# Optimization experiments

Hardware: AMD Instinct MI355X
Metric: run time of the kernel (lower is better)

The kernel has to match this reference:

```python
import jax, jax.numpy as jnp
import numpy as np

D_MODEL = 1024
D_STATE = 16
D_CONV = 4
EXPAND = 2
DT_RANK = 64
D_INNER = EXPAND * D_MODEL  # 2048
BATCH = 2
SEQ = 1024


def _silu(v):
    return v * jax.nn.sigmoid(v)


def setup_inputs() -> dict:
    key = jax.random.key(0)
    ks = jax.random.split(key, 8)
    x = jax.random.normal(ks[0], (BATCH, SEQ, D_MODEL), dtype=jnp.float32)
    W_in = jax.random.normal(ks[1], (2 * D_INNER, D_MODEL), dtype=jnp.float32) * (D_MODEL ** -0.5)
    conv_w = jax.random.normal(ks[2], (D_INNER, 1, D_CONV), dtype=jnp.float32) * (D_CONV ** -0.5)
    conv_b = jnp.zeros((D_INNER,), dtype=jnp.float32)
    W_x = jax.random.normal(ks[3], (DT_RANK + 2 * D_STATE, D_INNER), dtype=jnp.float32) * (D_INNER ** -0.5)
    W_dt = jax.random.uniform(ks[4], (D_INNER, DT_RANK), minval=-(DT_RANK ** -0.5), maxval=DT_RANK ** -0.5, dtype=jnp.float32)
    # dt bias init: inverse-softplus of dt sampled log-uniform in [1e-3, 1e-1]
    dt = jnp.exp(jax.random.uniform(ks[5], (D_INNER,), dtype=jnp.float32) * (np.log(0.1) - np.log(0.001)) + np.log(0.001))
    dt = jnp.clip(dt, 1e-4)
    b_dt = dt + jnp.log(-jnp.expm1(-dt))
    # A_log init: log of 1..d_state tiled per channel (S4D-real)
    A_log = jnp.log(jnp.tile(jnp.arange(1, D_STATE + 1, dtype=jnp.float32), (D_INNER, 1)))
    D = jnp.ones((D_INNER,), dtype=jnp.float32)
    W_out = jax.random.normal(ks[6], (D_MODEL, D_INNER), dtype=jnp.float32) * (D_INNER ** -0.5)
    return {"x": x, "W_in": W_in, "conv_w": conv_w, "conv_b": conv_b, "W_x": W_x,
            "W_dt": W_dt, "b_dt": b_dt, "A_log": A_log, "D": D, "W_out": W_out}


def _selective_scan(u, dt, A, B_in, C_in, D):
    # u, dt: [B,L,d_inner]; B_in, C_in: [B,L,d_state]; A: [d_inner,d_state]; D: [d_inner]
    Bsz = u.shape[0]

    def step(h, inp):
        u_t, dt_t, B_t, C_t = inp  # [B,d_inner], [B,d_inner], [B,d_state], [B,d_state]
        dA = jnp.exp(dt_t[:, :, None] * A)                     # [B,d_inner,d_state]
        h = dA * h + dt_t[:, :, None] * B_t[:, None, :] * u_t[:, :, None]
        y = jnp.einsum('bds,bs->bd', h, C_t)
        return h, y

    h0 = jnp.zeros((Bsz, D_INNER, D_STATE), dtype=u.dtype)
    xs = (u.transpose(1, 0, 2), dt.transpose(1, 0, 2),
          B_in.transpose(1, 0, 2), C_in.transpose(1, 0, 2))
    _, ys = jax.lax.scan(step, h0, xs)                          # ys: [L,B,d_inner]
    return ys.transpose(1, 0, 2) + u * D


def reference(x, W_in, conv_w, conv_b, W_x, W_dt, b_dt, A_log, D, W_out):
    # in_proj and gate split
    xz = x @ W_in.T                                            # [B,T,2*d_inner]
    x_in, z = jnp.split(xz, 2, axis=-1)
    # depthwise causal conv1d (left-pad d_conv-1, same as pad-both + slice :T)
    xi = x_in.transpose(0, 2, 1)                               # [B,d_inner,T]
    conv = jax.lax.conv_general_dilated(xi, conv_w, window_strides=(1,),
                                        padding=[(D_CONV - 1, 0)],
                                        feature_group_count=D_INNER)
    x_act = _silu(conv + conv_b[None, :, None]).transpose(0, 2, 1)  # [B,T,d_inner]
    # dt / B / C projections
    dbc = x_act @ W_x.T
    dt_lr, B_in, C_in = jnp.split(dbc, [DT_RANK, DT_RANK + D_STATE], axis=-1)
    dt = jax.nn.softplus(dt_lr @ W_dt.T + b_dt)                # [B,T,d_inner]
    A = -jnp.exp(A_log)                                        # [d_inner,d_state]
    y = _selective_scan(x_act, dt, A, B_in, C_in, D)
    y = y * _silu(z)
    return y @ W_out.T
```

## Files before the change

kernel.cpp:

```cpp
#include <hip/hip_runtime.h>
#include <math.h>

#define D_MODEL 1024
#define D_STATE 16
#define D_CONV  4
#define DT_RANK 64
#define D_INNER 2048
#define BATCH   2
#define SEQ     1024
#define BT      (BATCH*SEQ)
#define KSPLIT  16

typedef int   v4i __attribute__((ext_vector_type(4)));
typedef float v4f __attribute__((ext_vector_type(4)));
typedef short s8v __attribute__((ext_vector_type(8)));
typedef unsigned short u16;

template<int BM, int BN, int BK, int TM, int TN, int EPI>
__launch_bounds__(256)
__global__ void gemm_nt(const float* __restrict__ A, int lda,
                        const float* __restrict__ B, int ldb,
                        float* __restrict__ C, int ldc,
                        int K, const float* __restrict__ bias) {
    constexpr int BX = BN / TN;
    constexpr int BY = BM / TM;
    constexpr int THREADS = BX * BY;

    __shared__ float As[BK][BM + 1];
    __shared__ float Bs[BK][BN + 1];

    const int tid = threadIdx.x;
    const int tx  = tid % BX;
    const int ty  = tid / BX;
    const int m0  = blockIdx.y * BM;
    const int n0  = blockIdx.x * BN;

    float acc[TM][TN] = {};

    for (int k0 = 0; k0 < K; k0 += BK) {
        #pragma unroll
        for (int l = 0; l < (BM * BK) / (THREADS * 4); ++l) {
            int idx = (tid + l * THREADS) * 4;
            int row = idx / BK, col = idx % BK;
            const float4 v = *reinterpret_cast<const float4*>(
                &A[(size_t)(m0 + row) * lda + k0 + col]);
            As[col + 0][row] = v.x; As[col + 1][row] = v.y;
            As[col + 2][row] = v.z; As[col + 3][row] = v.w;
        }
        #pragma unroll
        for (int l = 0; l < (BN * BK) / (THREADS * 4); ++l) {
            int idx = (tid + l * THREADS) * 4;
            int row = idx / BK, col = idx % BK;
            const float4 v = *reinterpret_cast<const float4*>(
                &B[(size_t)(n0 + row) * ldb + k0 + col]);
            Bs[col + 0][row] = v.x; Bs[col + 1][row] = v.y;
            Bs[col + 2][row] = v.z; Bs[col + 3][row] = v.w;
        }
        __syncthreads();

        #pragma unroll
        for (int kk = 0; kk < BK; ++kk) {
            float a[TM], b[TN];
            #pragma unroll
            for (int i = 0; i < TM; ++i) a[i] = As[kk][ty * TM + i];
            #pragma unroll
            for (int j = 0; j < TN; ++j) b[j] = Bs[kk][tx * TN + j];
            #pragma unroll
            for (int i = 0; i < TM; ++i)
                #pragma unroll
                for (int j = 0; j < TN; ++j)
                    acc[i][j] = fmaf(a[i], b[j], acc[i][j]);
        }
        __syncthreads();
    }

    #pragma unroll
    for (int i = 0; i < TM; ++i) {
        float* outp = &C[(size_t)(m0 + ty * TM + i) * ldc + n0 + tx * TN];
        float vals[4];
        #pragma unroll
        for (int j = 0; j < TN; ++j) {
            float val = acc[i][j];
            if (EPI == 1) {
                val += bias[n0 + tx * TN + j];
                val = (val > 20.f) ? val : log1pf(expf(val));
            }
            vals[j] = val;
        }
        float4 v;
        v.x = vals[0]; v.y = vals[1]; v.z = vals[2]; v.w = vals[3];
        *reinterpret_cast<float4*>(outp) = v;
    }
}

template<int BM, int BN, int BK, int TM, int TN>
__launch_bounds__(128)
__global__ void gemm_nt_splitk(const float* __restrict__ A, int lda,
                               const float* __restrict__ B, int ldb,
                               float* __restrict__ part, int N, int kchunk) {
    constexpr int BX = BN / TN;
    constexpr int BY = BM / TM;
    constexpr int THREADS = BX * BY;

    __shared__ float As[BK][BM + 1];
    __shared__ float Bs[BK][BN + 1];

    const int tid = threadIdx.x;
    const int tx  = tid % BX;
    const int ty  = tid / BX;
    const int m0  = blockIdx.y * BM;
    const int n0  = blockIdx.x * BN;
    const int kb  = blockIdx.z * kchunk;

    float acc[TM][TN] = {};

    for (int k0 = kb; k0 < kb + kchunk; k0 += BK) {
        #pragma unroll
        for (int l = 0; l < (BM * BK) / (THREADS * 4); ++l) {
            int idx = (tid + l * THREADS) * 4;
            int row = idx / BK, col = idx % BK;
            const float4 v = *reinterpret_cast<const float4*>(
                &A[(size_t)(m0 + row) * lda + k0 + col]);
            As[col + 0][row] = v.x; As[col + 1][row] = v.y;
            As[col + 2][row] = v.z; As[col + 3][row] = v.w;
        }
        #pragma unroll
        for (int l = 0; l < (BN * BK) / (THREADS * 4); ++l) {
            int idx = (tid + l * THREADS) * 4;
            int row = idx / BK, col = idx % BK;
            const float4 v = *reinterpret_cast<const float4*>(
                &B[(size_t)(n0 + row) * ldb + k0 + col]);
            Bs[col + 0][row] = v.x; Bs[col + 1][row] = v.y;
            Bs[col + 2][row] = v.z; Bs[col + 3][row] = v.w;
        }
        __syncthreads();

        #pragma unroll
        for (int kk = 0; kk < BK; ++kk) {
            float a[TM], b[TN];
            #pragma unroll
            for (int i = 0; i < TM; ++i) a[i] = As[kk][ty * TM + i];
            #pragma unroll
            for (int j = 0; j < TN; ++j) b[j] = Bs[kk][tx * TN + j];
            #pragma unroll
            for (int i = 0; i < TM; ++i)
                #pragma unroll
                for (int j = 0; j < TN; ++j)
                    acc[i][j] = fmaf(a[i], b[j], acc[i][j]);
        }
        __syncthreads();
    }

    float* base = part + (size_t)blockIdx.z * BT * N;
    #pragma unroll
    for (int i = 0; i < TM; ++i) {
        float* outp = &base[(size_t)(m0 + ty * TM + i) * N + n0 + tx * TN];
        float4 v;
        v.x = acc[i][0]; v.y = acc[i][1]; v.z = acc[i][2]; v.w = acc[i][3];
        *reinterpret_cast<float4*>(outp) = v;
    }
}

__global__ void reduce_splitk(const float* __restrict__ part,
                              float* __restrict__ outp, int n) {
    const int idx = blockIdx.x * 256 + threadIdx.x;
    if (idx >= n) return;
    float s = 0.f;
    #pragma unroll
    for (int kc = 0; kc < KSPLIT; ++kc)
        s += part[(size_t)kc * n + idx];
    outp[idx] = s;
}

__device__ __forceinline__ u16 rne_bf16(float x) {
    unsigned int u = __float_as_uint(x);
    unsigned int r = u + 0x7FFFu + ((u >> 16) & 1u);
    return (u16)(r >> 16);
}

__global__ void prep_kernel(const float* __restrict__ x,
                            const float* __restrict__ Win,
                            const float* __restrict__ Wout,
                            u16* __restrict__ xh,
                            u16* __restrict__ winh, u16* __restrict__ wouth) {
    const size_t M2 = 2u * 1024u * 1024u;
    size_t i = ((size_t)blockIdx.x * 256 + threadIdx.x) * 8;
    const float* src;
    u16* dst;
    size_t j;
    if (i < M2)            { src = x;    dst = xh;    j = i; }
    else if (i < 3 * M2)   { src = Win;  dst = winh;  j = i - M2; }
    else                   { src = Wout; dst = wouth; j = i - 3 * M2; }
    float4 a = *reinterpret_cast<const float4*>(&src[j]);
    float4 b = *reinterpret_cast<const float4*>(&src[j + 4]);
    float xs[8] = {a.x, a.y, a.z, a.w, b.x, b.y, b.z, b.w};
    unsigned int hw[4];
    #pragma unroll
    for (int q = 0; q < 4; ++q)
        hw[q] = (unsigned int)rne_bf16(xs[2*q]) | ((unsigned int)rne_bf16(xs[2*q+1]) << 16);
    *reinterpret_cast<v4i*>(&dst[j]) = *reinterpret_cast<v4i*>(hw);
}

template<int BM, int BN, int WM, int WN>
__launch_bounds__(256)
__global__ void gemm_bf16(const u16* __restrict__ Ahi, int lda,
                          const u16* __restrict__ Bhi, int ldb,
                          float* __restrict__ C, int ldc, int K) {
    constexpr int ACH = BM / 64;
    constexpr int BCH = BN / 64;
    constexpr int WMF = WM / 16;
    constexpr int WNF = WN / 16;
    constexpr int SA  = BM * 40;
    constexpr int SB  = BN * 40;
    constexpr int BUFSZ = SA + SB;
    constexpr int WCOLS = BN / WN;

    __shared__ u16 smem[2 * BUFSZ];

    const int tid  = threadIdx.x;
    const int lane = tid & 63;
    const int wave = tid >> 6;
    const int wr   = wave / WCOLS, wc = wave % WCOLS;
    const int m0   = blockIdx.y * BM, n0 = blockIdx.x * BN;

    size_t aBase[ACH]; int aW[ACH];
    #pragma unroll
    for (int q = 0; q < ACH; ++q) {
        int c = tid + q * 256, row = c >> 2, slot = c & 3;
        aBase[q] = (size_t)(m0 + row) * lda + slot * 8;
        aW[q] = row * 40 + slot * 8;
    }
    size_t bBase[BCH]; int bW[BCH];
    #pragma unroll
    for (int q = 0; q < BCH; ++q) {
        int c = tid + q * 256, row = c >> 2, slot = c & 3;
        bBase[q] = (size_t)(n0 + row) * ldb + slot * 8;
        bW[q] = row * 40 + slot * 8;
    }

    const int fr = lane & 15;
    const int fk = (lane >> 4) * 8;
    const int fq = lane >> 4;
    int aOff[WMF], bOff[WNF];
    #pragma unroll
    for (int i = 0; i < WMF; ++i) aOff[i] = (wr * WM + i * 16 + fr) * 40 + fk;
    #pragma unroll
    for (int j = 0; j < WNF; ++j) bOff[j] = (wc * WN + j * 16 + fr) * 40 + fk;

    v4f acc[WMF][WNF];
    #pragma unroll
    for (int i = 0; i < WMF; ++i)
        #pragma unroll
        for (int j = 0; j < WNF; ++j)
            acc[i][j] = (v4f)0.f;

    v4i rA[ACH], rB[BCH];

    auto loadg = [&](int k0) {
        #pragma unroll
        for (int q = 0; q < ACH; ++q)
            rA[q] = *reinterpret_cast<const v4i*>(Ahi + aBase[q] + k0);
        #pragma unroll
        for (int q = 0; q < BCH; ++q)
            rB[q] = *reinterpret_cast<const v4i*>(Bhi + bBase[q] + k0);
    };
    auto writelds = [&](u16* buf) {
        #pragma unroll
        for (int q = 0; q < ACH; ++q)
            *reinterpret_cast<v4i*>(&buf[aW[q]]) = rA[q];
        #pragma unroll
        for (int q = 0; q < BCH; ++q)
            *reinterpret_cast<v4i*>(&buf[SA + bW[q]]) = rB[q];
    };

    const int NK = K / 32;
    loadg(0);
    writelds(smem);
    if (NK > 1) loadg(32);
    __syncthreads();

    for (int k = 0; k < NK; ++k) {
        u16* cur = smem + (k & 1) * BUFSZ;
        if (k + 1 < NK) {
            writelds(smem + ((k + 1) & 1) * BUFSZ);
            if (k + 2 < NK) loadg((k + 2) * 32);
        }

        s8v ah[WMF];
        #pragma unroll
        for (int i = 0; i < WMF; ++i)
            ah[i] = *reinterpret_cast<const s8v*>(&cur[aOff[i]]);
        #pragma unroll
        for (int j = 0; j < WNF; ++j) {
            const s8v bh = *reinterpret_cast<const s8v*>(&cur[SA + bOff[j]]);
            #pragma unroll
            for (int i = 0; i < WMF; ++i)
                acc[i][j] = __builtin_amdgcn_mfma_f32_16x16x32_bf16(ah[i], bh, acc[i][j], 0, 0, 0);
        }
        __syncthreads();
    }

    #pragma unroll
    for (int i = 0; i < WMF; ++i) {
        const int row = m0 + wr * WM + i * 16 + fq * 4;
        #pragma unroll
        for (int j = 0; j < WNF; ++j) {
            const int col = n0 + wc * WN + j * 16 + fr;
            #pragma unroll
            for (int r = 0; r < 4; ++r)
                C[(size_t)(row + r) * ldc + col] = acc[i][j][r];
        }
    }
}

__global__ void conv_silu_kernel(const float* __restrict__ x_in, int xld,
                                 const float* __restrict__ w,
                                 const float* __restrict__ b,
                                 float* __restrict__ x_act) {
    const int idx = blockIdx.x * blockDim.x + threadIdx.x;
    const int ch4 = (idx * 4) % D_INNER;
    const int m   = (idx * 4) / D_INNER;
    const int t   = m % SEQ;

    float4 wrow[4];
    #pragma unroll
    for (int c = 0; c < 4; ++c)
        wrow[c] = *reinterpret_cast<const float4*>(&w[(ch4 + c) * D_CONV]);
    float4 acc = *reinterpret_cast<const float4*>(&b[ch4]);

    #pragma unroll
    for (int j = 0; j < D_CONV; ++j) {
        const int tt = t - (D_CONV - 1) + j;
        if (tt >= 0) {
            const float4 xi = *reinterpret_cast<const float4*>(
                &x_in[(size_t)(m - (D_CONV - 1) + j) * xld + ch4]);
            acc.x = fmaf(((const float*)&wrow[0])[j], xi.x, acc.x);
            acc.y = fmaf(((const float*)&wrow[1])[j], xi.y, acc.y);
            acc.z = fmaf(((const float*)&wrow[2])[j], xi.z, acc.z);
            acc.w = fmaf(((const float*)&wrow[3])[j], xi.w, acc.w);
        }
    }
    acc.x = acc.x / (1.f + __expf(-acc.x));
    acc.y = acc.y / (1.f + __expf(-acc.y));
    acc.z = acc.z / (1.f + __expf(-acc.z));
    acc.w = acc.w / (1.f + __expf(-acc.w));
    *reinterpret_cast<float4*>(&x_act[(size_t)idx * 4]) = acc;
}

template<int NC>
__launch_bounds__(256)
__global__ void scan_part1(const float* __restrict__ dt,
                           const float* __restrict__ x_act,
                           const float* __restrict__ dbc,
                           const float* __restrict__ A_log,
                           float* __restrict__ P, float* __restrict__ F) {
    constexpr int CL = SEQ / NC;
    __shared__ float Bsh[CL][D_STATE];
    const int tid = threadIdx.x;
    const int d = blockIdx.x * 256 + tid;
    const int c = blockIdx.y;
    const int b = blockIdx.z;
    const int mbase = b * SEQ + c * CL;

    {
        const int s = tid & 15, t0 = tid >> 4;
        #pragma unroll
        for (int q = 0; q < CL / 16; ++q)
            Bsh[t0 + 16 * q][s] = dbc[(size_t)(mbase + t0 + 16 * q) * 96 + DT_RANK + s];
    }
    float A[16];
    #pragma unroll
    for (int q = 0; q < 4; ++q) {
        float4 v = *reinterpret_cast<const float4*>(&A_log[d * 16 + q * 4]);
        A[q*4+0] = -__expf(v.x); A[q*4+1] = -__expf(v.y);
        A[q*4+2] = -__expf(v.z); A[q*4+3] = -__expf(v.w);
    }
    __syncthreads();

    float h[16] = {};
    float Pp[16];
    #pragma unroll
    for (int s = 0; s < 16; ++s) Pp[s] = 1.f;

    for (int t = 0; t < CL; ++t) {
        const int m = mbase + t;
        const float dtv = dt[(size_t)m * D_INNER + d];
        const float u   = x_act[(size_t)m * D_INNER + d];
        const float du  = dtv * u;
        float Bv[16];
        #pragma unroll
        for (int q = 0; q < 4; ++q) {
            float4 v = *reinterpret_cast<const float4*>(&Bsh[t][q * 4]);
            Bv[q*4+0] = v.x; Bv[q*4+1] = v.y; Bv[q*4+2] = v.z; Bv[q*4+3] = v.w;
        }
        #pragma unroll
        for (int s = 0; s < 16; ++s) {
            const float dA = __expf(dtv * A[s]);
            Pp[s] *= dA;
            h[s] = fmaf(dA, h[s], du * Bv[s]);
        }
    }
    const size_t base = ((size_t)(b * NC + c) * 16) * D_INNER + d;
    #pragma unroll
    for (int s = 0; s < 16; ++s) {
        P[base + (size_t)s * D_INNER] = Pp[s];
        F[base + (size_t)s * D_INNER] = h[s];
    }
}

template<int NC>
__launch_bounds__(256, 2)
__global__ void scan_combine(const float* __restrict__ P, float* F) {
    const int idx = blockIdx.x * 256 + threadIdx.x;
    const int d  = idx % D_INNER;
    const int bs = idx / D_INNER;
    const int b  = bs >> 4, s = bs & 15;
    const size_t base0 = ((size_t)b * NC * 16 + s) * D_INNER + d;
    const size_t cstep = (size_t)16 * D_INNER;

    float Pv[NC], Fv[NC];
    #pragma unroll
    for (int c = 0; c < NC; ++c) {
        Pv[c] = P[base0 + c * cstep];
        Fv[c] = F[base0 + c * cstep];
    }
    float G = 0.f;
    #pragma unroll
    for (int c = 0; c < NC; ++c) {
        const float f = Fv[c];
        Fv[c] = G;
        G = fmaf(Pv[c], G, f);
    }
    #pragma unroll
    for (int c = 0; c < NC; ++c)
        F[base0 + c * cstep] = Fv[c];
}

template<int NC, int BF16OUT>
__launch_bounds__(256)
__global__ void scan_part2(const float* __restrict__ dt,
                           const float* __restrict__ x_act,
                           const float* __restrict__ dbc,
                           const float* __restrict__ A_log,
                           const float* __restrict__ Dp,
                           const float* __restrict__ Ginit,
                           const float* zp, int zld,
                           float* yf, u16* yh) {
    constexpr int CL = SEQ / NC;
    __shared__ float BCs[CL][32];
    const int tid = threadIdx.x;
    const int d = blockIdx.x * 256 + tid;
    const int c = blockIdx.y;
    const int b = blockIdx.z;
    const int mbase = b * SEQ + c * CL;

    {
        const int t0 = tid >> 3;
        const int j  = (tid & 7) * 4;
        if (t0 < CL) {
            float4 v = *reinterpret_cast<const float4*>(
                &dbc[(size_t)(mbase + t0) * 96 + DT_RANK + j]);
            *reinterpret_cast<float4*>(&BCs[t0][j]) = v;
        }
    }
    float A[16];
    #pragma unroll
    for (int q = 0; q < 4; ++q) {
        float4 v = *reinterpret_cast<const float4*>(&A_log[d * 16 + q * 4]);
        A[q*4+0] = -__expf(v.x); A[q*4+1] = -__expf(v.y);
        A[q*4+2] = -__expf(v.z); A[q*4+3] = -__expf(v.w);
    }
    float h[16];
    const size_t gbase = ((size_t)(b * NC + c) * 16) * D_INNER + d;
    #pragma unroll
    for (int s = 0; s < 16; ++s) h[s] = Ginit[gbase + (size_t)s * D_INNER];
    const float Dv = Dp[d];
    __syncthreads();

    for (int half = 0; half < 2; ++half) {
        const int tb = half * (CL / 2);
        float zreg[CL / 2];
        #pragma unroll
        for (int t = 0; t < CL / 2; ++t)
            zreg[t] = zp[(size_t)(mbase + tb + t) * zld + d];

        for (int t = 0; t < CL / 2; ++t) {
            const int m = mbase + tb + t;
            const float dtv = dt[(size_t)m * D_INNER + d];
            const float u   = x_act[(size_t)m * D_INNER + d];
            const float du  = dtv * u;
            float Bv[16], Cv[16];
            #pragma unroll
            for (int q = 0; q < 4; ++q) {
                float4 vb = *reinterpret_cast<const float4*>(&BCs[tb + t][q * 4]);
                float4 vc = *reinterpret_cast<const float4*>(&BCs[tb + t][16 + q * 4]);
                Bv[q*4+0] = vb.x; Bv[q*4+1] = vb.y; Bv[q*4+2] = vb.z; Bv[q*4+3] = vb.w;
                Cv[q*4+0] = vc.x; Cv[q*4+1] = vc.y; Cv[q*4+2] = vc.z; Cv[q*4+3] = vc.w;
            }
            float y0 = 0.f, y1 = 0.f;
            #pragma unroll
            for (int s = 0; s < 16; s += 2) {
                const float dA0 = __expf(dtv * A[s]);
                const float dA1 = __expf(dtv * A[s + 1]);
                h[s]     = fmaf(dA0, h[s],     du * Bv[s]);
                h[s + 1] = fmaf(dA1, h[s + 1], du * Bv[s + 1]);
                y0 = fmaf(h[s],     Cv[s],     y0);
                y1 = fmaf(h[s + 1], Cv[s + 1], y1);
            }
            float y = y0 + y1;
            y = fmaf(u, Dv, y);
            const float zv = zreg[t];
            const float g  = zv / (1.f + __expf(-zv));
            const float val = y * g;
            if (BF16OUT) {
                yh[(size_t)m * D_INNER + d] = rne_bf16(val);
            } else {
                yf[(size_t)m * D_INNER + d] = val;
            }
        }
    }
}

extern "C" void kernel_launch(void* const* d_in, const int* in_sizes, int n_in,
                              void* d_out, int out_size, void* d_ws, size_t ws_size,
                              hipStream_t stream) {
    const float* x      = (const float*)d_in[0];
    const float* W_in   = (const float*)d_in[1];
    const float* conv_w = (const float*)d_in[2];
    const float* conv_b = (const float*)d_in[3];
    const float* W_x    = (const float*)d_in[4];
    const float* W_dt   = (const float*)d_in[5];
    const float* b_dt   = (const float*)d_in[6];
    const float* A_log  = (const float*)d_in[7];
    const float* Dp     = (const float*)d_in[8];
    const float* W_out  = (const float*)d_in[9];
    float* out = (float*)d_out;

    const size_t M1 = 1024u * 1024u;
    const size_t fXZ = 8 * M1, fXACT = 4 * M1, fDBC = (size_t)BT * 96,
                 fDT = 4 * M1;
    const size_t fPF32 = 2 * M1;
    const size_t fPF64 = 4 * M1;
    const size_t shorts = 12 * M1;
    const size_t need32 = (fXZ + fXACT + fDBC + fDT + 2 * fPF32) * 4 + shorts * 2;
    const size_t need64 = (fXZ + fXACT + fDBC + fDT + 2 * fPF64) * 4 + shorts * 2;

    if (ws_size >= need32) {
        const bool big = (ws_size >= need64);
        const size_t fPF = big ? fPF64 : fPF32;

        float* ws    = (float*)d_ws;
        float* xz    = ws;
        float* x_act = xz    + fXZ;
        float* dbc   = x_act + fXACT;
        float* dtbuf = dbc   + fDBC;
        float* Pbuf  = dtbuf + fDT;
        float* Fbuf  = Pbuf  + fPF;
        u16* xh    = (u16*)(Fbuf + fPF);
        u16* winh  = xh    + 2 * M1;
        u16* wouth = winh  + 4 * M1;
        u16* yh    = wouth + 2 * M1;
        float* dbc_part = Pbuf;

        prep_kernel<<<dim3((8 * M1) / 2048), 256, 0, stream>>>(
            x, W_in, W_out, xh, winh, wouth);

        gemm_bf16<128, 128, 64, 64><<<dim3(4096 / 128, BT / 128), 256, 0, stream>>>(
            xh, D_MODEL, winh, D_MODEL, xz, 4096, D_MODEL);

        conv_silu_kernel<<<dim3((BT * D_INNER) / 1024), 256, 0, stream>>>(
            xz, 4096, conv_w, conv_b, x_act);

        gemm_nt_splitk<64,32,16,4,4><<<dim3(96 / 32, BT / 64, KSPLIT), 128, 0, stream>>>(
            x_act, D_INNER, W_x, D_INNER, dbc_part, 96, D_INNER / KSPLIT);
        reduce_splitk<<<dim3((BT * 96 + 255) / 256), 256, 0, stream>>>(
            dbc_part, dbc, BT * 96);

        gemm_nt<64,64,16,4,4,1><<<dim3(D_INNER / 64, BT / 64), 256, 0, stream>>>(
            dbc, 96, W_dt, DT_RANK, dtbuf, D_INNER, DT_RANK, b_dt);

        if (big) {
            scan_part1<64><<<dim3(D_INNER / 256, 64, BATCH), 256, 0, stream>>>(
                dtbuf, x_act, dbc, A_log, Pbuf, Fbuf);
            scan_combine<64><<<dim3((BATCH * 16 * D_INNER) / 256), 256, 0, stream>>>(
                Pbuf, Fbuf);
            scan_part2<64, 1><<<dim3(D_INNER / 256, 64, BATCH), 256, 0, stream>>>(
                dtbuf, x_act, dbc, A_log, Dp, Fbuf, xz + D_INNER, 4096,
                nullptr, yh);
        } else {
            scan_part1<32><<<dim3(D_INNER / 256, 32, BATCH), 256, 0, stream>>>(
                dtbuf, x_act, dbc, A_log, Pbuf, Fbuf);
            scan_combine<32><<<dim3((BATCH * 16 * D_INNER) / 256), 256, 0, stream>>>(
                Pbuf, Fbuf);
            scan_part2<32, 1><<<dim3(D_INNER / 256, 32, BATCH), 256, 0, stream>>>(
                dtbuf, x_act, dbc, A_log, Dp, Fbuf, xz + D_INNER, 4096,
                nullptr, yh);
        }

        gemm_bf16<64, 128, 32, 64><<<dim3(D_MODEL / 128, BT / 64), 256, 0, stream>>>(
            yh, D_INNER, wouth, D_INNER, out, D_MODEL, D_INNER);
    } else {
        float* ws    = (float*)d_ws;
        float* x_in  = ws;
        float* z     = x_in  + (size_t)BT * D_INNER;
        float* x_act = z     + (size_t)BT * D_INNER;
        float* dbc   = x_act + (size_t)BT * D_INNER;
        float* Pbuf  = dbc   + (size_t)BT * 96;
        float* Fbuf  = Pbuf  + (size_t)BATCH * 32 * 16 * D_INNER;
        float* dtbuf = x_in;
        float* yf    = z;

        gemm_nt<64,64,16,4,4,0><<<dim3(D_INNER/64, BT/64), 256, 0, stream>>>(
            x, D_MODEL, W_in, D_MODEL, x_in, D_INNER, D_MODEL, nullptr);
        gemm_nt<64,64,16,4,4,0><<<dim3(D_INNER/64, BT/64), 256, 0, stream>>>(
            x, D_MODEL, W_in + (size_t)D_INNER * D_MODEL, D_MODEL, z, D_INNER, D_MODEL, nullptr);
        conv_silu_kernel<<<dim3((BT * D_INNER) / 1024), 256, 0, stream>>>(
            x_in, D_INNER, conv_w, conv_b, x_act);
        gemm_nt<64,32,16,4,4,0><<<dim3(96/32, BT/64), 128, 0, stream>>>(
            x_act, D_INNER, W_x, D_INNER, dbc, 96, D_INNER, nullptr);
        gemm_nt<64,64,16,4,4,1><<<dim3(D_INNER/64, BT/64), 256, 0, stream>>>(
            dbc, 96, W_dt, DT_RANK, dtbuf, D_INNER, DT_RANK, b_dt);
        scan_part1<32><<<dim3(D_INNER/256, 32, BATCH), 256, 0, stream>>>(
            dtbuf, x_act, dbc, A_log, Pbuf, Fbuf);
        scan_combine<32><<<dim3((BATCH * 16 * D_INNER) / 256), 256, 0, stream>>>(
            Pbuf, Fbuf);
        scan_part2<32, 0><<<dim3(D_INNER/256, 32, BATCH), 256, 0, stream>>>(
            dtbuf, x_act, dbc, A_log, Dp, Fbuf, z, D_INNER, yf, nullptr);
        gemm_nt<64,64,16,4,4,0><<<dim3(D_MODEL/64, BT/64), 256, 0, stream>>>(
            yf, D_INNER, W_out, D_INNER, out, D_MODEL, D_INNER, nullptr);
    }
}
```

Before: 181.8 us.

## Fuse fp32-to-bf16 conversion into GEMM loads and store xz as bf16

Removes the separate prep kernel. The in_proj and out_proj GEMMs now read fp32 operands directly and pack them to bf16 in registers with v_cvt_pk_bf16_f32 before writing to LDS. The in_proj GEMM also writes its xz output as bf16, and the conv and scan kernels read that bf16 buffer. This cuts a kernel launch and a full conversion pass, halves the xz traffic, and shrinks the workspace. In exchange the GEMMs issue twice the global load bytes per tile, and z and x_in lose precision from being stored in bf16.

```diff
diff --git a/kernel.cpp b/kernel.cpp
--- a/kernel.cpp
+++ b/kernel.cpp
@@ -177,35 +177,24 @@
     unsigned int r = u + 0x7FFFu + ((u >> 16) & 1u);
     return (u16)(r >> 16);
 }
-
-__global__ void prep_kernel(const float* __restrict__ x,
-                            const float* __restrict__ Win,
-                            const float* __restrict__ Wout,
-                            u16* __restrict__ xh,
-                            u16* __restrict__ winh, u16* __restrict__ wouth) {
-    const size_t M2 = 2u * 1024u * 1024u;
-    size_t i = ((size_t)blockIdx.x * 256 + threadIdx.x) * 8;
-    const float* src;
-    u16* dst;
-    size_t j;
-    if (i < M2)            { src = x;    dst = xh;    j = i; }
-    else if (i < 3 * M2)   { src = Win;  dst = winh;  j = i - M2; }
-    else                   { src = Wout; dst = wouth; j = i - 3 * M2; }
-    float4 a = *reinterpret_cast<const float4*>(&src[j]);
-    float4 b = *reinterpret_cast<const float4*>(&src[j + 4]);
-    float xs[8] = {a.x, a.y, a.z, a.w, b.x, b.y, b.z, b.w};
-    unsigned int hw[4];
-    #pragma unroll
-    for (int q = 0; q < 4; ++q)
-        hw[q] = (unsigned int)rne_bf16(xs[2*q]) | ((unsigned int)rne_bf16(xs[2*q+1]) << 16);
-    *reinterpret_cast<v4i*>(&dst[j]) = *reinterpret_cast<v4i*>(hw);
-}
-
-template<int BM, int BN, int WM, int WN>
+__device__ __forceinline__ float bf2f(u16 h) {
+    return __uint_as_float((unsigned int)h << 16);
+}
+__device__ __forceinline__ v4i pack8_bf16(const float4& a, const float4& b) {
+    unsigned int r0, r1, r2, r3;
+    asm("v_cvt_pk_bf16_f32 %0, %1, %2" : "=v"(r0) : "v"(a.x), "v"(a.y));
+    asm("v_cvt_pk_bf16_f32 %0, %1, %2" : "=v"(r1) : "v"(a.z), "v"(a.w));
+    asm("v_cvt_pk_bf16_f32 %0, %1, %2" : "=v"(r2) : "v"(b.x), "v"(b.y));
+    asm("v_cvt_pk_bf16_f32 %0, %1, %2" : "=v"(r3) : "v"(b.z), "v"(b.w));
+    v4i r; r[0] = (int)r0; r[1] = (int)r1; r[2] = (int)r2; r[3] = (int)r3;
+    return r;
+}
+
+template<int BM, int BN, int WM, int WN, int AF32, int BF32, int CBF16>
 __launch_bounds__(256)
-__global__ void gemm_bf16(const u16* __restrict__ Ahi, int lda,
-                          const u16* __restrict__ Bhi, int ldb,
-                          float* __restrict__ C, int ldc, int K) {
+__global__ void gemm_mx(const void* __restrict__ Ap, int lda,
+                        const void* __restrict__ Bp, int ldb,
+                        void* __restrict__ Cp, int ldc, int K) {
     constexpr int ACH = BM / 64;
     constexpr int BCH = BN / 64;
     constexpr int WMF = WM / 16;
@@ -254,23 +243,52 @@
         for (int j = 0; j < WNF; ++j)
             acc[i][j] = (v4f)0.f;
 
-    v4i rA[ACH], rB[BCH];
+    float4 rAf[ACH][2]; v4i rA[ACH];
+    float4 rBf[BCH][2]; v4i rB[BCH];
 
     auto loadg = [&](int k0) {
-        #pragma unroll
-        for (int q = 0; q < ACH; ++q)
-            rA[q] = *reinterpret_cast<const v4i*>(Ahi + aBase[q] + k0);
-        #pragma unroll
-        for (int q = 0; q < BCH; ++q)
-            rB[q] = *reinterpret_cast<const v4i*>(Bhi + bBase[q] + k0);
+        if constexpr (AF32) {
+            const float* A = (const float*)Ap;
+            #pragma unroll
+            for (int q = 0; q < ACH; ++q) {
+                rAf[q][0] = *reinterpret_cast<const float4*>(A + aBase[q] + k0);
+                rAf[q][1] = *reinterpret_cast<const float4*>(A + aBase[q] + k0 + 4);
+            }
+        } else {
+            const u16* A = (const u16*)Ap;
+            #pragma unroll
+            for (int q = 0; q < ACH; ++q)
+                rA[q] = *reinterpret_cast<const v4i*>(A + aBase[q] + k0);
+        }
+        if constexpr (BF32) {
+            const float* B = (const float*)Bp;
+            #pragma unroll
+            for (int q = 0; q < BCH; ++q) {
+                rBf[q][0] = *reinterpret_cast<const float4*>(B + bBase[q] + k0);
+                rBf[q][1] = *reinterpret_cast<const float4*>(B + bBase[q] + k0 + 4);
+            }
+        } else {
+            const u16* B = (const u16*)Bp;
+            #pragma unroll
+            for (int q = 0; q < BCH; ++q)
+                rB[q] = *reinterpret_cast<const v4i*>(B + bBase[q] + k0);
+        }
     };
     auto writelds = [&](u16* buf) {
         #pragma unroll
-        for (int q = 0; q < ACH; ++q)
-            *reinterpret_cast<v4i*>(&buf[aW[q]]) = rA[q];
-        #pragma unroll
-        for (int q = 0; q < BCH; ++q)
-            *reinterpret_cast<v4i*>(&buf[SA + bW[q]]) = rB[q];
+        for (int q = 0; q < ACH; ++q) {
+            v4i v;
+            if constexpr (AF32) v = pack8_bf16(rAf[q][0], rAf[q][1]);
+            else v = rA[q];
+            *reinterpret_cast<v4i*>(&buf[aW[q]]) = v;
+        }
+        #pragma unroll
+        for (int q = 0; q < BCH; ++q) {
+            v4i v;
+            if constexpr (BF32) v = pack8_bf16(rBf[q][0], rBf[q][1]);
+            else v = rB[q];
+            *reinterpret_cast<v4i*>(&buf[SA + bW[q]]) = v;
+        }
     };
 
     const int NK = K / 32;
@@ -307,13 +325,19 @@
         for (int j = 0; j < WNF; ++j) {
             const int col = n0 + wc * WN + j * 16 + fr;
             #pragma unroll
-            for (int r = 0; r < 4; ++r)
-                C[(size_t)(row + r) * ldc + col] = acc[i][j][r];
-        }
-    }
-}
-
-__global__ void conv_silu_kernel(const float* __restrict__ x_in, int xld,
+            for (int r = 0; r < 4; ++r) {
+                if constexpr (CBF16) {
+                    ((u16*)Cp)[(size_t)(row + r) * ldc + col] = rne_bf16(acc[i][j][r]);
+                } else {
+                    ((float*)Cp)[(size_t)(row + r) * ldc + col] = acc[i][j][r];
+                }
+            }
+        }
+    }
+}
+
+template<int INBF16>
+__global__ void conv_silu_kernel(const void* __restrict__ x_in, int xld,
                                  const float* __restrict__ w,
                                  const float* __restrict__ b,
                                  float* __restrict__ x_act) {
@@ -332,12 +356,21 @@
     for (int j = 0; j < D_CONV; ++j) {
         const int tt = t - (D_CONV - 1) + j;
         if (tt >= 0) {
-            const float4 xi = *reinterpret_cast<const float4*>(
-                &x_in[(size_t)(m - (D_CONV - 1) + j) * xld + ch4]);
-            acc.x = fmaf(((const float*)&wrow[0])[j], xi.x, acc.x);
-            acc.y = fmaf(((const float*)&wrow[1])[j], xi.y, acc.y);
-            acc.z = fmaf(((const float*)&wrow[2])[j], xi.z, acc.z);
-            acc.w = fmaf(((const float*)&wrow[3])[j], xi.w, acc.w);
+            float xi[4];
+            if (INBF16) {
+                const ushort4 v = *reinterpret_cast<const ushort4*>(
+                    &((const u16*)x_in)[(size_t)(m - (D_CONV - 1) + j) * xld + ch4]);
+                xi[0] = bf2f(v.x); xi[1] = bf2f(v.y);
+                xi[2] = bf2f(v.z); xi[3] = bf2f(v.w);
+            } else {
+                const float4 v = *reinterpret_cast<const float4*>(
+                    &((const float*)x_in)[(size_t)(m - (D_CONV - 1) + j) * xld + ch4]);
+                xi[0] = v.x; xi[1] = v.y; xi[2] = v.z; xi[3] = v.w;
+            }
+            acc.x = fmaf(((const float*)&wrow[0])[j], xi[0], acc.x);
+            acc.y = fmaf(((const float*)&wrow[1])[j], xi[1], acc.y);
+            acc.z = fmaf(((const float*)&wrow[2])[j], xi[2], acc.z);
+            acc.w = fmaf(((const float*)&wrow[3])[j], xi[3], acc.w);
         }
     }
     acc.x = acc.x / (1.f + __expf(-acc.x));
@@ -436,7 +469,7 @@
         F[base0 + c * cstep] = Fv[c];
 }
 
-template<int NC, int BF16OUT>
+template<int NC, int ZBF16, int BF16OUT>
 __launch_bounds__(256)
 __global__ void scan_part2(const float* __restrict__ dt,
                            const float* __restrict__ x_act,
@@ -444,7 +477,7 @@
                            const float* __restrict__ A_log,
                            const float* __restrict__ Dp,
                            const float* __restrict__ Ginit,
-                           const float* zp, int zld,
+                           const void* zp, int zld,
                            float* yf, u16* yh) {
     constexpr int CL = SEQ / NC;
     __shared__ float BCs[CL][32];
@@ -481,8 +514,12 @@
         const int tb = half * (CL / 2);
         float zreg[CL / 2];
         #pragma unroll
-        for (int t = 0; t < CL / 2; ++t)
-            zreg[t] = zp[(size_t)(mbase + tb + t) * zld + d];
+        for (int t = 0; t < CL / 2; ++t) {
+            if (ZBF16)
+                zreg[t] = bf2f(((const u16*)zp)[(size_t)(mbase + tb + t) * zld + d]);
+            else
+                zreg[t] = ((const float*)zp)[(size_t)(mbase + tb + t) * zld + d];
+        }
 
         for (int t = 0; t < CL / 2; ++t) {
             const int m = mbase + tb + t;
@@ -537,38 +574,31 @@
     float* out = (float*)d_out;
 
     const size_t M1 = 1024u * 1024u;
-    const size_t fXZ = 8 * M1, fXACT = 4 * M1, fDBC = (size_t)BT * 96,
-                 fDT = 4 * M1;
+    const size_t fXACT = 4 * M1, fDBC = (size_t)BT * 96, fDT = 4 * M1;
     const size_t fPF32 = 2 * M1;
     const size_t fPF64 = 4 * M1;
     const size_t shorts = 12 * M1;
-    const size_t need32 = (fXZ + fXACT + fDBC + fDT + 2 * fPF32) * 4 + shorts * 2;
-    const size_t need64 = (fXZ + fXACT + fDBC + fDT + 2 * fPF64) * 4 + shorts * 2;
+    const size_t need32 = (fXACT + fDBC + fDT + 2 * fPF32) * 4 + shorts * 2;
+    const size_t need64 = (fXACT + fDBC + fDT + 2 * fPF64) * 4 + shorts * 2;
 
     if (ws_size >= need32) {
         const bool big = (ws_size >= need64);
         const size_t fPF = big ? fPF64 : fPF32;
 
         float* ws    = (float*)d_ws;
-        float* xz    = ws;
-        float* x_act = xz    + fXZ;
+        float* x_act = ws;
         float* dbc   = x_act + fXACT;
         float* dtbuf = dbc   + fDBC;
         float* Pbuf  = dtbuf + fDT;
         float* Fbuf  = Pbuf  + fPF;
-        u16* xh    = (u16*)(Fbuf + fPF);
-        u16* winh  = xh    + 2 * M1;
-        u16* wouth = winh  + 4 * M1;
-        u16* yh    = wouth + 2 * M1;
+        u16* xz = (u16*)(Fbuf + fPF);
+        u16* yh = xz + 8 * M1;
         float* dbc_part = Pbuf;
 
-        prep_kernel<<<dim3((8 * M1) / 2048), 256, 0, stream>>>(
-            x, W_in, W_out, xh, winh, wouth);
-
-        gemm_bf16<128, 128, 64, 64><<<dim3(4096 / 128, BT / 128), 256, 0, stream>>>(
-            xh, D_MODEL, winh, D_MODEL, xz, 4096, D_MODEL);
-
-        conv_silu_kernel<<<dim3((BT * D_INNER) / 1024), 256, 0, stream>>>(
+        gemm_mx<128, 128, 64, 64, 1, 1, 1><<<dim3(4096 / 128, BT / 128), 256, 0, stream>>>(
+            x, D_MODEL, W_in, D_MODEL, xz, 4096, D_MODEL);
+
+        conv_silu_kernel<1><<<dim3((BT * D_INNER) / 1024), 256, 0, stream>>>(
             xz, 4096, conv_w, conv_b, x_act);
 
         gemm_nt_splitk<64,32,16,4,4><<<dim3(96 / 32, BT / 64, KSPLIT), 128, 0, stream>>>(
@@ -584,7 +614,7 @@
                 dtbuf, x_act, dbc, A_log, Pbuf, Fbuf);
             scan_combine<64><<<dim3((BATCH * 16 * D_INNER) / 256), 256, 0, stream>>>(
                 Pbuf, Fbuf);
-            scan_part2<64, 1><<<dim3(D_INNER / 256, 64, BATCH), 256, 0, stream>>>(
+            scan_part2<64, 1, 1><<<dim3(D_INNER / 256, 64, BATCH), 256, 0, stream>>>(
                 dtbuf, x_act, dbc, A_log, Dp, Fbuf, xz + D_INNER, 4096,
                 nullptr, yh);
         } else {
@@ -592,13 +622,13 @@
                 dtbuf, x_act, dbc, A_log, Pbuf, Fbuf);
             scan_combine<32><<<dim3((BATCH * 16 * D_INNER) / 256), 256, 0, stream>>>(
                 Pbuf, Fbuf);
-            scan_part2<32, 1><<<dim3(D_INNER / 256, 32, BATCH), 256, 0, stream>>>(
+            scan_part2<32, 1, 1><<<dim3(D_INNER / 256, 32, BATCH), 256, 0, stream>>>(
                 dtbuf, x_act, dbc, A_log, Dp, Fbuf, xz + D_INNER, 4096,
                 nullptr, yh);
         }
 
-        gemm_bf16<64, 128, 32, 64><<<dim3(D_MODEL / 128, BT / 64), 256, 0, stream>>>(
-            yh, D_INNER, wouth, D_INNER, out, D_MODEL, D_INNER);
+        gemm_mx<64, 128, 32, 64, 0, 1, 0><<<dim3(D_MODEL / 128, BT / 64), 256, 0, stream>>>(
+            yh, D_INNER, W_out, D_INNER, out, D_MODEL, D_INNER);
     } else {
         float* ws    = (float*)d_ws;
         float* x_in  = ws;
@@ -614,7 +644,7 @@
             x, D_MODEL, W_in, D_MODEL, x_in, D_INNER, D_MODEL, nullptr);
         gemm_nt<64,64,16,4,4,0><<<dim3(D_INNER/64, BT/64), 256, 0, stream>>>(
             x, D_MODEL, W_in + (size_t)D_INNER * D_MODEL, D_MODEL, z, D_INNER, D_MODEL, nullptr);
-        conv_silu_kernel<<<dim3((BT * D_INNER) / 1024), 256, 0, stream>>>(
+        conv_silu_kernel<0><<<dim3((BT * D_INNER) / 1024), 256, 0, stream>>>(
             x_in, D_INNER, conv_w, conv_b, x_act);
         gemm_nt<64,32,16,4,4,0><<<dim3(96/32, BT/64), 128, 0, stream>>>(
             x_act, D_INNER, W_x, D_INNER, dbc, 96, D_INNER, nullptr);
@@ -624,7 +654,7 @@
             dtbuf, x_act, dbc, A_log, Pbuf, Fbuf);
         scan_combine<32><<<dim3((BATCH * 16 * D_INNER) / 256), 256, 0, stream>>>(
             Pbuf, Fbuf);
-        scan_part2<32, 0><<<dim3(D_INNER/256, 32, BATCH), 256, 0, stream>>>(
+        scan_part2<32, 0, 0><<<dim3(D_INNER/256, 32, BATCH), 256, 0, stream>>>(
             dtbuf, x_act, dbc, A_log, Dp, Fbuf, z, D_INNER, yf, nullptr);
         gemm_nt<64,64,16,4,4,0><<<dim3(D_MODEL/64, BT/64), 256, 0, stream>>>(
             yf, D_INNER, W_out, D_INNER, out, D_MODEL, D_INNER, nullptr);
```

After: 178.7 us. Within noise of the previous version (-1.7%).
